# Kernel optimization log

Hardware: AMD Instinct MI355X
Metric: run time of the kernel (lower is better)

Reference implementation:

```python
import jax, jax.numpy as jnp
import numpy as np

B, S, D, H = 2, 2048, 1024, 16
Dh = D // H

def setup_inputs() -> dict:
    key = jax.random.key(0)
    ks = jax.random.split(key, 11)
    def lin(k, fan_in):
        bound = 1.0 / np.sqrt(fan_in)
        kw, kb = jax.random.split(k)
        W = jax.random.uniform(kw, (D, D), jnp.float32, -bound, bound)
        b = jax.random.uniform(kb, (D,), jnp.float32, -bound, bound)
        return W, b
    Wq, bq = lin(ks[0], D)
    Wk, bk = lin(ks[1], D)
    Wv, bv = lin(ks[2], D)
    Wo, bo = lin(ks[3], D)
    Q = jax.random.normal(ks[4], (B, S, D), jnp.float32)
    K = jax.random.normal(ks[5], (B, S, D), jnp.float32)
    V = jax.random.normal(ks[6], (B, S, D), jnp.float32)
    return {"Q": Q, "K": K, "V": V, "Wq": Wq, "bq": bq, "Wk": Wk, "bk": bk,
            "Wv": Wv, "bv": bv, "Wo": Wo, "bo": bo}

def _split_heads(x):
    # [B,S,D] -> [B,H,S,Dh]
    b, s, _ = x.shape
    return x.reshape(b, s, H, Dh).transpose(0, 2, 1, 3)

def reference(Q, K, V, Wq, bq, Wk, bk, Wv, bv, Wo, bo):
    q = _split_heads(Q @ Wq.T + bq)
    k = _split_heads(K @ Wk.T + bk)
    v = _split_heads(V @ Wv.T + bv)
    scores = jnp.einsum('bhqd,bhkd->bhqk', q, k) / jnp.sqrt(jnp.float32(Dh))
    attn = jax.nn.softmax(scores, axis=-1)
    out = jnp.einsum('bhqk,bhkd->bhqd', attn, v)  # [B,H,S,Dh]
    out = out.transpose(0, 2, 1, 3).reshape(Q.shape[0], Q.shape[1], D)
    return out @ Wo.T + bo
```

## Files before the change

kernel.cpp:

```cpp
#include <hip/hip_runtime.h>

#define SEQ 2048
#define DMODEL 1024
#define NH 16
#define DH 64

typedef __attribute__((ext_vector_type(8))) short bf16x8;
typedef __attribute__((ext_vector_type(4))) short bf16x4;
typedef __attribute__((ext_vector_type(4))) float floatx4;
typedef __attribute__((ext_vector_type(4))) unsigned short u16x4;
typedef unsigned short u16;
typedef unsigned int u32;

typedef const void __attribute__((address_space(1)))* as1cvp;
typedef void __attribute__((address_space(3)))* as3vp;

__device__ __forceinline__ void glds16(const void* g, void* l) {
    __builtin_amdgcn_global_load_lds((as1cvp)g, (as3vp)l, 16, 0, 0);
}

__device__ __forceinline__ u16 f2bf(float f) {
    union { u32 u; float f; } v; v.f = f;
    return (u16)((v.u + 0x8000u) >> 16);
}

__device__ __forceinline__ u32 pk2(float a, float b) {
    union { u32 u; float f; } x, y; x.f = a; y.f = b;
    u32 xr = x.u + 0x8000u, yr = y.u + 0x8000u;
#if __has_builtin(__builtin_amdgcn_perm)
    return __builtin_amdgcn_perm(yr, xr, 0x07060302u);
#else
    return (xr >> 16) | (yr & 0xffff0000u);
#endif
}

__device__ __forceinline__ float ex2(float x) {
#if __has_builtin(__builtin_amdgcn_exp2f)
    return __builtin_amdgcn_exp2f(x);
#else
    float r; asm("v_exp_f32 %0, %1" : "=v"(r) : "v"(x)); return r;
#endif
}

__device__ __forceinline__ floatx4 mfma32(bf16x8 a, bf16x8 b, floatx4 c) {
    return __builtin_amdgcn_mfma_f32_16x16x32_bf16(a, b, c, 0, 0, 0);
}

__device__ __forceinline__ uint4 cvt8(const float* __restrict__ p) {
    float4 a = *(const float4*)p;
    float4 b = *(const float4*)(p + 4);
    uint4 q;
    q.x = pk2(a.x, a.y); q.y = pk2(a.z, a.w);
    q.z = pk2(b.x, b.y); q.w = pk2(b.z, b.w);
    return q;
}

#define QSCALE 0.18033688011112042f

__global__ __launch_bounds__(256) void cvt_all(
    const float* __restrict__ Q, const float* __restrict__ K, const float* __restrict__ V,
    const float* __restrict__ W0, const float* __restrict__ W1,
    const float* __restrict__ W2, const float* __restrict__ W3,
    u16* __restrict__ Qb, u16* __restrict__ Kb, u16* __restrict__ Vb,
    u16* __restrict__ Wb)
{
    const int y = blockIdx.y;
    const float* src; u16* dst;
    if (y == 0)      { src = Q;  dst = Qb; }
    else if (y == 1) { src = K;  dst = Kb; }
    else if (y == 2) { src = V;  dst = Vb; }
    else {
        if (blockIdx.x >= 512) return;
        src = (y == 3) ? W0 : (y == 4) ? W1 : (y == 5) ? W2 : W3;
        dst = Wb + (size_t)(y - 3) * 1048576;
    }
    size_t i = ((size_t)blockIdx.x * 256 + threadIdx.x) * 8;
    *(uint4*)(dst + i) = cvt8(src + i);
}

__global__ __launch_bounds__(256) void cvt_w(
    const float* __restrict__ W0, const float* __restrict__ W1,
    const float* __restrict__ W2, const float* __restrict__ W3,
    u16* __restrict__ out)
{
    const float* src = (blockIdx.y == 0) ? W0 : (blockIdx.y == 1) ? W1
                     : (blockIdx.y == 2) ? W2 : W3;
    size_t i = ((size_t)blockIdx.x * 256 + threadIdx.x) * 8;
    *(uint4*)(out + (size_t)blockIdx.y * 1048576 + i) = cvt8(src + i);
}

__device__ __forceinline__ void qkv_store(
    int z, u16* __restrict__ outp, int rowg, int col, floatx4 a4, float bv, float sc)
{
    union { u32 w[2]; u16 h[4]; u16x4 v4; } pk;
    pk.w[0] = pk2((a4[0] + bv) * sc, (a4[1] + bv) * sc);
    pk.w[1] = pk2((a4[2] + bv) * sc, (a4[3] + bv) * sc);
    int b = rowg >> 11, s = rowg & 2047, h = col >> 6, d = col & 63;
    if (z < 2) {
#pragma unroll
        for (int r = 0; r < 4; r++)
            outp[((size_t)(b * NH + h) * SEQ + s + r) * DH + d] = pk.h[r];
    } else {
        *(u16x4*)(outp + ((size_t)(b * NH + h) * DH + d) * SEQ + s) = pk.v4;
    }
}

__global__ __launch_bounds__(256) void gemm_qkv_bb(
    const u16* __restrict__ Qb, const u16* __restrict__ Kb, const u16* __restrict__ Vb,
    const u16* __restrict__ Wb,
    const float* __restrict__ b0, const float* __restrict__ b1, const float* __restrict__ b2,
    u16* __restrict__ qo, u16* __restrict__ ko, u16* __restrict__ vto)
{
    __shared__ __align__(16) u16 As[3][4096];
    __shared__ __align__(16) u16 Bs[3][4096];
    const int tid = threadIdx.x, l = tid & 63, w = tid >> 6;
    const int lm = l & 15, quad = l >> 4;
    const int wr = (w >> 1) * 64, wc = (w & 1) * 64;
    const int bm = blockIdx.y * 128, bn = blockIdx.x * 128;
    const int z = blockIdx.z;
    const u16* A      = (z == 0) ? Qb : (z == 1) ? Kb : Vb;
    const u16* W      = Wb + (size_t)z * 1048576;
    const float* bias = (z == 0) ? b0 : (z == 1) ? b1 : b2;

    const int srow = tid >> 2, scol = (tid & 3) * 8;

    floatx4 acc[4][4];
#pragma unroll
    for (int i = 0; i < 4; i++)
#pragma unroll
        for (int j = 0; j < 4; j++) acc[i][j] = (floatx4){0.f, 0.f, 0.f, 0.f};

#define QKV_STAGE(I, NB) do { \
        const int kt_ = (I) * 32; \
        glds16(A + (size_t)(bm + srow) * DMODEL + kt_ + scol, As[NB] + w * 512); \
        glds16(A + (size_t)(bm + 64 + srow) * DMODEL + kt_ + scol, As[NB] + 2048 + w * 512); \
        glds16(W + (size_t)(bn + srow) * DMODEL + kt_ + scol, Bs[NB] + w * 512); \
        glds16(W + (size_t)(bn + 64 + srow) * DMODEL + kt_ + scol, Bs[NB] + 2048 + w * 512); \
    } while (0)

    QKV_STAGE(0, 0);
    QKV_STAGE(1, 1);
    asm volatile("s_waitcnt vmcnt(4)" ::: "memory");
    __builtin_amdgcn_s_barrier();

    int cur = 0, nx = 2;
    for (int i = 0; i < 32; i++) {
        bf16x8 af[4], bfr[4];
#pragma unroll
        for (int mi = 0; mi < 4; mi++)
            af[mi] = *(const bf16x8*)(As[cur] + (wr + mi * 16 + lm) * 32 + quad * 8);
#pragma unroll
        for (int ni = 0; ni < 4; ni++)
            bfr[ni] = *(const bf16x8*)(Bs[cur] + (wc + ni * 16 + lm) * 32 + quad * 8);
#pragma unroll
        for (int mi = 0; mi < 4; mi++)
#pragma unroll
            for (int ni = 0; ni < 4; ni++)
                acc[mi][ni] = __builtin_amdgcn_mfma_f32_16x16x32_bf16(
                    af[mi], bfr[ni], acc[mi][ni], 0, 0, 0);

        if (i + 2 < 32) {
            QKV_STAGE(i + 2, nx);
            asm volatile("s_waitcnt vmcnt(4)" ::: "memory");
            __builtin_amdgcn_s_barrier();
        } else if (i + 1 < 32) {
            asm volatile("s_waitcnt vmcnt(0)" ::: "memory");
            __builtin_amdgcn_s_barrier();
        }
        cur = (cur == 2) ? 0 : cur + 1;
        nx  = (nx == 2) ? 0 : nx + 1;
    }
#undef QKV_STAGE

    const float sc = (z == 0) ? QSCALE : 1.0f;
    u16* outp = (z == 0) ? qo : (z == 1) ? ko : vto;
#pragma unroll
    for (int ni = 0; ni < 4; ni++) {
        int col = bn + wc + ni * 16 + lm;
        float bv = bias[col];
#pragma unroll
        for (int mi = 0; mi < 4; mi++)
            qkv_store(z, outp, bm + wr + mi * 16 + quad * 4, col, acc[mi][ni], bv, sc);
    }
}

template<bool WBF>
__global__ __launch_bounds__(256) void gemm_qkv(
    const float* __restrict__ Qf, const float* __restrict__ Kf, const float* __restrict__ Vf,
    const void* __restrict__ W0, const void* __restrict__ W1, const void* __restrict__ W2,
    const float* __restrict__ b0, const float* __restrict__ b1, const float* __restrict__ b2,
    u16* __restrict__ qo, u16* __restrict__ ko, u16* __restrict__ vto)
{
    __shared__ __align__(16) u16 As[128 * 32];
    __shared__ __align__(16) u16 Bs[128 * 32];
    const int tid = threadIdx.x, l = tid & 63, w = tid >> 6;
    const int lm = l & 15, quad = l >> 4;
    const int wr = (w >> 1) * 64, wc = (w & 1) * 64;
    const int bm = blockIdx.y * 128, bn = blockIdx.x * 128;
    const int z = blockIdx.z;
    const float* A    = (z == 0) ? Qf : (z == 1) ? Kf : Vf;
    const void* Wp    = (z == 0) ? W0 : (z == 1) ? W1 : W2;
    const float* bias = (z == 0) ? b0 : (z == 1) ? b1 : b2;

    floatx4 acc[4][4];
#pragma unroll
    for (int i = 0; i < 4; i++)
#pragma unroll
        for (int j = 0; j < 4; j++) acc[i][j] = (floatx4){0.f, 0.f, 0.f, 0.f};

    for (int kt = 0; kt < DMODEL; kt += 32) {
        __syncthreads();
#pragma unroll
        for (int j = 0; j < 2; j++) {
            int ch = j * 256 + tid, row = ch >> 2, c = ch & 3;
            *(uint4*)(As + ch * 8) = cvt8(A + (size_t)(bm + row) * DMODEL + kt + c * 8);
        }
        if (WBF) {
            const u16* Wc = (const u16*)Wp;
            glds16(Wc + (size_t)(bn + (tid >> 2)) * DMODEL + kt + (tid & 3) * 8, Bs + w * 512);
            glds16(Wc + (size_t)(bn + 64 + (tid >> 2)) * DMODEL + kt + (tid & 3) * 8, Bs + 2048 + w * 512);
        } else {
            const float* Wf = (const float*)Wp;
#pragma unroll
            for (int j = 0; j < 2; j++) {
                int ch = j * 256 + tid, row = ch >> 2, c = ch & 3;
                *(uint4*)(Bs + ch * 8) = cvt8(Wf + (size_t)(bn + row) * DMODEL + kt + c * 8);
            }
        }
        __syncthreads();

        bf16x8 af[4], bfr[4];
#pragma unroll
        for (int mi = 0; mi < 4; mi++)
            af[mi] = *(const bf16x8*)(As + (wr + mi * 16 + lm) * 32 + quad * 8);
#pragma unroll
        for (int ni = 0; ni < 4; ni++)
            bfr[ni] = *(const bf16x8*)(Bs + (wc + ni * 16 + lm) * 32 + quad * 8);
#pragma unroll
        for (int mi = 0; mi < 4; mi++)
#pragma unroll
            for (int ni = 0; ni < 4; ni++)
                acc[mi][ni] = __builtin_amdgcn_mfma_f32_16x16x32_bf16(
                    af[mi], bfr[ni], acc[mi][ni], 0, 0, 0);
    }

    const float sc = (z == 0) ? QSCALE : 1.0f;
    u16* outp = (z == 0) ? qo : (z == 1) ? ko : vto;
#pragma unroll
    for (int ni = 0; ni < 4; ni++) {
        int col = bn + wc + ni * 16 + lm;
        float bv = bias[col];
#pragma unroll
        for (int mi = 0; mi < 4; mi++)
            qkv_store(z, outp, bm + wr + mi * 16 + quad * 4, col, acc[mi][ni], bv, sc);
    }
}

__global__ __launch_bounds__(256) void gemm_o_p(
    const u16* __restrict__ A, const u16* __restrict__ W,
    const float* __restrict__ bias, float* __restrict__ out)
{
    __shared__ __align__(16) u16 As[3][4096];
    __shared__ __align__(16) u16 Bs[3][2048];
    const int tid = threadIdx.x, l = tid & 63, w = tid >> 6;
    const int lm = l & 15, quad = l >> 4;
    const int bm = blockIdx.y * 128, bn = blockIdx.x * 64;

    floatx4 acc[2][4];
#pragma unroll
    for (int i = 0; i < 2; i++)
#pragma unroll
        for (int j = 0; j < 4; j++) acc[i][j] = (floatx4){0.f, 0.f, 0.f, 0.f};

#define O_STAGE(I, NB) do { \
        const int kt_ = (I) * 32; \
        glds16(A + (size_t)(bm + (tid >> 2)) * DMODEL + kt_ + (tid & 3) * 8, As[NB] + w * 512); \
        glds16(A + (size_t)(bm + 64 + (tid >> 2)) * DMODEL + kt_ + (tid & 3) * 8, As[NB] + 2048 + w * 512); \
        glds16(W + (size_t)(bn + (tid >> 2)) * DMODEL + kt_ + (tid & 3) * 8, Bs[NB] + w * 512); \
    } while (0)

    O_STAGE(0, 0);
    O_STAGE(1, 1);
    asm volatile("s_waitcnt vmcnt(3)" ::: "memory");
    __builtin_amdgcn_s_barrier();

    int cur = 0, nx = 2;
    for (int i = 0; i < 32; i++) {
        bf16x8 af[2], bfr[4];
#pragma unroll
        for (int mi = 0; mi < 2; mi++)
            af[mi] = *(const bf16x8*)(As[cur] + (w * 32 + mi * 16 + lm) * 32 + quad * 8);
#pragma unroll
        for (int ni = 0; ni < 4; ni++)
            bfr[ni] = *(const bf16x8*)(Bs[cur] + (ni * 16 + lm) * 32 + quad * 8);
#pragma unroll
        for (int mi = 0; mi < 2; mi++)
#pragma unroll
            for (int ni = 0; ni < 4; ni++)
                acc[mi][ni] = __builtin_amdgcn_mfma_f32_16x16x32_bf16(
                    af[mi], bfr[ni], acc[mi][ni], 0, 0, 0);

        if (i + 2 < 32) {
            O_STAGE(i + 2, nx);
            asm volatile("s_waitcnt vmcnt(3)" ::: "memory");
            __builtin_amdgcn_s_barrier();
        } else if (i + 1 < 32) {
            asm volatile("s_waitcnt vmcnt(0)" ::: "memory");
            __builtin_amdgcn_s_barrier();
        }
        cur = (cur == 2) ? 0 : cur + 1;
        nx  = (nx == 2) ? 0 : nx + 1;
    }
#undef O_STAGE

#pragma unroll
    for (int ni = 0; ni < 4; ni++) {
        int col = bn + ni * 16 + lm;
        float bv = bias[col];
#pragma unroll
        for (int mi = 0; mi < 2; mi++) {
#pragma unroll
            for (int r = 0; r < 4; r++) {
                int rowg = bm + w * 32 + mi * 16 + quad * 4 + r;
                out[(size_t)rowg * DMODEL + col] = acc[mi][ni][r] + bv;
            }
        }
    }
}

template<bool WBF>
__global__ __launch_bounds__(256) void gemm_o(
    const u16* __restrict__ A, const void* __restrict__ Wp,
    const float* __restrict__ bias, float* __restrict__ out)
{
    __shared__ __align__(16) u16 As[128 * 32];
    __shared__ __align__(16) u16 Bs[64 * 32];
    const int tid = threadIdx.x, l = tid & 63, w = tid >> 6;
    const int lm = l & 15, quad = l >> 4;
    const int bm = blockIdx.y * 128, bn = blockIdx.x * 64;

    floatx4 acc[2][4];
#pragma unroll
    for (int i = 0; i < 2; i++)
#pragma unroll
        for (int j = 0; j < 4; j++) acc[i][j] = (floatx4){0.f, 0.f, 0.f, 0.f};

    for (int kt = 0; kt < DMODEL; kt += 32) {
        __syncthreads();
        glds16(A + (size_t)(bm + (tid >> 2)) * DMODEL + kt + (tid & 3) * 8, As + w * 512);
        glds16(A + (size_t)(bm + 64 + (tid >> 2)) * DMODEL + kt + (tid & 3) * 8, As + 2048 + w * 512);
        if (WBF) {
            glds16((const u16*)Wp + (size_t)(bn + (tid >> 2)) * DMODEL + kt + (tid & 3) * 8, Bs + w * 512);
        } else {
            *(uint4*)(Bs + tid * 8) =
                cvt8((const float*)Wp + (size_t)(bn + (tid >> 2)) * DMODEL + kt + (tid & 3) * 8);
        }
        __syncthreads();

        bf16x8 af[2], bfr[4];
#pragma unroll
        for (int mi = 0; mi < 2; mi++)
            af[mi] = *(const bf16x8*)(As + (w * 32 + mi * 16 + lm) * 32 + quad * 8);
#pragma unroll
        for (int ni = 0; ni < 4; ni++)
            bfr[ni] = *(const bf16x8*)(Bs + (ni * 16 + lm) * 32 + quad * 8);
#pragma unroll
        for (int mi = 0; mi < 2; mi++)
#pragma unroll
            for (int ni = 0; ni < 4; ni++)
                acc[mi][ni] = __builtin_amdgcn_mfma_f32_16x16x32_bf16(
                    af[mi], bfr[ni], acc[mi][ni], 0, 0, 0);
    }

#pragma unroll
    for (int ni = 0; ni < 4; ni++) {
        int col = bn + ni * 16 + lm;
        float bv = bias[col];
#pragma unroll
        for (int mi = 0; mi < 2; mi++) {
#pragma unroll
            for (int r = 0; r < 4; r++) {
                int rowg = bm + w * 32 + mi * 16 + quad * 4 + r;
                out[(size_t)rowg * DMODEL + col] = acc[mi][ni][r] + bv;
            }
        }
    }
}

#define SP 72
#define TS (64 * SP)
#define BUFSZ (4 * TS)
__global__ __launch_bounds__(256, 2) void attn_kernel(
    const u16* __restrict__ q, const u16* __restrict__ k,
    const u16* __restrict__ vt, u16* __restrict__ out)
{
    __shared__ __align__(16) u16 smem[2 * BUFSZ];
    const int tid = threadIdx.x, l = tid & 63, w = tid >> 6;
    const int lm = l & 15, quad = l >> 4;
    const int qt = blockIdx.x, bh = blockIdx.y;
    const int b = bh >> 4, h = bh & 15;
    const int rg = w & 1, half = w >> 1;

    bf16x8 qf[4][2];
#pragma unroll
    for (int nt = 0; nt < 4; nt++) {
        int row = qt * 128 + rg * 64 + nt * 16 + lm;
        const u16* qp = q + ((size_t)bh * SEQ + row) * DH;
        qf[nt][0] = *(const bf16x8*)(qp + quad * 8);
        qf[nt][1] = *(const bf16x8*)(qp + 32 + quad * 8);
    }

    floatx4 O[4][4];
#pragma unroll
    for (int dt = 0; dt < 4; dt++)
#pragma unroll
        for (int nt = 0; nt < 4; nt++) O[dt][nt] = (floatx4){0.f, 0.f, 0.f, 0.f};
    floatx4 Ol[4];
#pragma unroll
    for (int nt = 0; nt < 4; nt++) Ol[nt] = (floatx4){0.f, 0.f, 0.f, 0.f};

    const bf16x8 ones8 = {(short)0x3F80, (short)0x3F80, (short)0x3F80, (short)0x3F80,
                          (short)0x3F80, (short)0x3F80, (short)0x3F80, (short)0x3F80};

    const int srow = tid >> 2, sc4 = tid & 3;
    const int prow = (srow & 32) | ((srow & 4) << 2) | ((srow & 24) >> 1) | (srow & 3);
    const u16* kbase = k + (size_t)bh * SEQ * DH;
    const u16* vbase = vt + (size_t)bh * DH * SEQ;

    uint4 kA0, kA1, kB0, kB1, vA0, vA1, vB0, vB1;
#define LOADT(T) do { \
        const u16* kgA = kbase + (size_t)((T) * 64 + srow) * DH + sc4 * 16; \
        const u16* kgB = kbase + (size_t)(1024 + (T) * 64 + srow) * DH + sc4 * 16; \
        kA0 = *(const uint4*)kgA;       kA1 = *(const uint4*)(kgA + 8); \
        kB0 = *(const uint4*)kgB;       kB1 = *(const uint4*)(kgB + 8); \
        const u16* vgA = vbase + (size_t)srow * SEQ + (T) * 64 + sc4 * 16; \
        const u16* vgB = vgA + 1024; \
        vA0 = *(const uint4*)vgA;       vA1 = *(const uint4*)(vgA + 8); \
        vB0 = *(const uint4*)vgB;       vB1 = *(const uint4*)(vgB + 8); \
    } while (0)
#define WRBUF(BUF) do { \
        u16* K0 = smem + (BUF) * BUFSZ; \
        u16* K1 = K0 + TS; \
        u16* V0 = K0 + 2 * TS; \
        u16* V1 = K0 + 3 * TS; \
        *(uint4*)(K0 + prow * SP + sc4 * 16)     = kA0; \
        *(uint4*)(K0 + prow * SP + sc4 * 16 + 8) = kA1; \
        *(uint4*)(K1 + prow * SP + sc4 * 16)     = kB0; \
        *(uint4*)(K1 + prow * SP + sc4 * 16 + 8) = kB1; \
        *(uint4*)(V0 + srow * SP + sc4 * 16)     = vA0; \
        *(uint4*)(V0 + srow * SP + sc4 * 16 + 8) = vA1; \
        *(uint4*)(V1 + srow * SP + sc4 * 16)     = vB0; \
        *(uint4*)(V1 + srow * SP + sc4 * 16 + 8) = vB1; \
    } while (0)

    LOADT(0);
    WRBUF(0);
    LOADT(1);
    asm volatile("s_waitcnt lgkmcnt(0)" ::: "memory");
    __builtin_amdgcn_s_barrier();

    for (int t = 0; t < 16; t++) {
        const int cur = t & 1;
        const u16* Kh = smem + cur * BUFSZ + half * TS;
        const u16* Vh = smem + cur * BUFSZ + (2 + half) * TS;

        floatx4 Sc[4][4];
        __builtin_amdgcn_s_setprio(1);
#pragma unroll
        for (int sub = 0; sub < 4; sub++) {
            bf16x8 ka0 = *(const bf16x8*)(Kh + (sub * 16 + lm) * SP + quad * 8);
            bf16x8 ka1 = *(const bf16x8*)(Kh + (sub * 16 + lm) * SP + 32 + quad * 8);
#pragma unroll
            for (int nt = 0; nt < 4; nt++) {
                floatx4 c = (floatx4){0.f, 0.f, 0.f, 0.f};
                c = mfma32(ka0, qf[nt][0], c);
                c = mfma32(ka1, qf[nt][1], c);
                Sc[sub][nt] = c;
            }
        }
        __builtin_amdgcn_s_setprio(0);

        if (t + 1 < 16) {
            asm volatile("s_waitcnt vmcnt(0)" ::: "memory");
            WRBUF(cur ^ 1);
            if (t + 2 < 16) LOADT(t + 2);
        }

        bf16x8 pbm[2][4];
#pragma unroll
        for (int p = 0; p < 2; p++)
#pragma unroll
            for (int nt = 0; nt < 4; nt++) {
                floatx4 sa = Sc[p * 2][nt], sb = Sc[p * 2 + 1][nt];
#pragma unroll
                for (int r = 0; r < 4; r++) { sa[r] = ex2(sa[r]); sb[r] = ex2(sb[r]); }
                union { u32 w4[4]; bf16x8 v; } pku;
                pku.w4[0] = pk2(sa[0], sa[1]);
                pku.w4[1] = pk2(sa[2], sa[3]);
                pku.w4[2] = pk2(sb[0], sb[1]);
                pku.w4[3] = pk2(sb[2], sb[3]);
                pbm[p][nt] = pku.v;
            }

        __builtin_amdgcn_s_setprio(1);
#pragma unroll
        for (int nt = 0; nt < 4; nt++) {
            Ol[nt] = mfma32(ones8, pbm[0][nt], Ol[nt]);
            Ol[nt] = mfma32(ones8, pbm[1][nt], Ol[nt]);
        }

#pragma unroll
        for (int dt = 0; dt < 4; dt++) {
            bf16x8 va0 = *(const bf16x8*)(Vh + (dt * 16 + lm) * SP + quad * 8);
            bf16x8 va1 = *(const bf16x8*)(Vh + (dt * 16 + lm) * SP + 32 + quad * 8);
#pragma unroll
            for (int nt = 0; nt < 4; nt++) {
                O[dt][nt] = mfma32(va0, pbm[0][nt], O[dt][nt]);
                O[dt][nt] = mfma32(va1, pbm[1][nt], O[dt][nt]);
            }
        }
        __builtin_amdgcn_s_setprio(0);

        asm volatile("s_waitcnt lgkmcnt(0)" ::: "memory");
        __builtin_amdgcn_s_barrier();
    }
#undef LOADT
#undef WRBUF

    float* obuf  = (float*)smem;
    float* mlbuf = (float*)smem + 8704;
    if (w >= 2) {
        float* ob = obuf + (rg * 64 + l) * 68;
        float* ml = mlbuf + (rg * 64 + l) * 5;
#pragma unroll
        for (int nt = 0; nt < 4; nt++) {
#pragma unroll
            for (int dt = 0; dt < 4; dt++)
                *(floatx4*)(ob + nt * 16 + dt * 4) = O[dt][nt];
            ml[nt] = Ol[nt][0];
        }
    }
    __syncthreads();
    if (w < 2) {
        float* ob = obuf + (rg * 64 + l) * 68;
        float* ml = mlbuf + (rg * 64 + l) * 5;
#pragma unroll
        for (int nt = 0; nt < 4; nt++) {
            float lB = ml[nt];
            float inv = 1.0f / (Ol[nt][0] + lB);
            int s = qt * 128 + rg * 64 + nt * 16 + lm;
            u16* op = out + ((size_t)b * SEQ + s) * DMODEL + h * DH;
#pragma unroll
            for (int dt = 0; dt < 4; dt++) {
                floatx4 Ob = *(const floatx4*)(ob + nt * 16 + dt * 4);
                union { u32 w2[2]; u16x4 v; } pku;
                pku.w2[0] = pk2((O[dt][nt][0] + Ob[0]) * inv,
                                (O[dt][nt][1] + Ob[1]) * inv);
                pku.w2[1] = pk2((O[dt][nt][2] + Ob[2]) * inv,
                                (O[dt][nt][3] + Ob[3]) * inv);
                *(u16x4*)(op + dt * 16 + quad * 4) = pku.v;
            }
        }
    }
}

extern "C" void kernel_launch(void* const* d_in, const int* in_sizes, int n_in,
                              void* d_out, int out_size, void* d_ws, size_t ws_size,
                              hipStream_t stream) {
    (void)in_sizes; (void)n_in; (void)out_size;
    const float* Q  = (const float*)d_in[0];
    const float* K  = (const float*)d_in[1];
    const float* V  = (const float*)d_in[2];
    const float* Wq = (const float*)d_in[3];
    const float* bq = (const float*)d_in[4];
    const float* Wk = (const float*)d_in[5];
    const float* bk = (const float*)d_in[6];
    const float* Wv = (const float*)d_in[7];
    const float* bv = (const float*)d_in[8];
    const float* Wo = (const float*)d_in[9];
    const float* bo = (const float*)d_in[10];

    const size_t NEL = (size_t)2 * NH * SEQ * DH;
    u16* base = (u16*)d_ws;
    dim3 bb(256);
    dim3 ab(256);

    if (ws_size >= 8 * NEL * 2) {
        u16* Qb   = base;
        u16* Kb   = Qb + NEL;
        u16* Vb   = Kb + NEL;
        u16* Wb   = Vb + NEL;
        u16* qws  = Wb + NEL;
        u16* kws  = qws + NEL;
        u16* vtws = kws + NEL;
        u16* aws  = vtws + NEL;
        cvt_all<<<dim3(2048, 7), bb, 0, stream>>>(Q, K, V, Wq, Wk, Wv, Wo, Qb, Kb, Vb, Wb);
        gemm_qkv_bb<<<dim3(8, 32, 3), bb, 0, stream>>>(
            Qb, Kb, Vb, Wb, bq, bk, bv, qws, kws, vtws);
        attn_kernel<<<dim3(SEQ / 128, 2 * NH), ab, 0, stream>>>(qws, kws, vtws, aws);
        gemm_o_p<<<dim3(16, 32), bb, 0, stream>>>(aws, Wb + 3145728, bo, (float*)d_out);
    } else if (ws_size >= 5 * NEL * 2) {
        u16* Wb = base;
        u16* qws = base + NEL; u16* kws = qws + NEL; u16* vtws = kws + NEL; u16* aws = vtws + NEL;
        cvt_w<<<dim3(512, 4), bb, 0, stream>>>(Wq, Wk, Wv, Wo, Wb);
        gemm_qkv<true><<<dim3(8, 32, 3), bb, 0, stream>>>(
            Q, K, V, Wb, Wb + 1048576, Wb + 2097152, bq, bk, bv, qws, kws, vtws);
        attn_kernel<<<dim3(SEQ / 128, 2 * NH), ab, 0, stream>>>(qws, kws, vtws, aws);
        gemm_o_p<<<dim3(16, 32), bb, 0, stream>>>(aws, Wb + 3145728, bo, (float*)d_out);
    } else {
        u16* qws = base; u16* kws = qws + NEL; u16* vtws = kws + NEL; u16* aws = vtws + NEL;
        gemm_qkv<false><<<dim3(8, 32, 3), bb, 0, stream>>>(
            Q, K, V, Wq, Wk, Wv, bq, bk, bv, qws, kws, vtws);
        attn_kernel<<<dim3(SEQ / 128, 2 * NH), ab, 0, stream>>>(qws, kws, vtws, aws);
        gemm_o<false><<<dim3(16, 32), bb, 0, stream>>>(aws, Wo, bo, (float*)d_out);
    }
}
```

Before: 218.7 us.

## Halve attention KV tile to 32 keys and raise occupancy to four blocks per CU

Shrinks each key/value tile per pipeline stage from 64 to 32 keys, which halves the shared-memory buffers and the S/P register arrays, and doubles the loop trip count to 32. The launch bound is raised from 2 to 4 blocks per CU to use the freed LDS and registers for more waves in flight, hiding latency. The cost is twice as many barriers and global-load rounds per block, with less MFMA work between each synchronization.

Result: slower. 484.9 us (+121.7%).

```diff
diff --git a/kernel.cpp b/kernel.cpp
--- a/kernel.cpp
+++ b/kernel.cpp
@@ -387,10 +387,13 @@
     }
 }
 
-#define SP 72
-#define TS (64 * SP)
-#define BUFSZ (4 * TS)
-__global__ __launch_bounds__(256, 2) void attn_kernel(
+#define KSP 72
+#define VSP 40
+#define KSZ (32 * KSP)
+#define VSZ (64 * VSP)
+#define BUFSZ (2 * KSZ + 2 * VSZ)
+#define NT 32
+__global__ __launch_bounds__(256, 4) void attn_kernel(
     const u16* __restrict__ q, const u16* __restrict__ k,
     const u16* __restrict__ vt, u16* __restrict__ out)
 {
@@ -422,35 +425,25 @@
     const bf16x8 ones8 = {(short)0x3F80, (short)0x3F80, (short)0x3F80, (short)0x3F80,
                           (short)0x3F80, (short)0x3F80, (short)0x3F80, (short)0x3F80};
 
-    const int srow = tid >> 2, sc4 = tid & 3;
-    const int prow = (srow & 32) | ((srow & 4) << 2) | ((srow & 24) >> 1) | (srow & 3);
+    const int krow = tid >> 3, kc = tid & 7;
+    const int vrow = tid >> 2, vc = tid & 3;
+    const int prow = ((krow & 4) << 2) | ((krow & 24) >> 1) | (krow & 3);
     const u16* kbase = k + (size_t)bh * SEQ * DH;
     const u16* vbase = vt + (size_t)bh * DH * SEQ;
 
-    uint4 kA0, kA1, kB0, kB1, vA0, vA1, vB0, vB1;
+    uint4 kA, kB, vA, vB;
 #define LOADT(T) do { \
-        const u16* kgA = kbase + (size_t)((T) * 64 + srow) * DH + sc4 * 16; \
-        const u16* kgB = kbase + (size_t)(1024 + (T) * 64 + srow) * DH + sc4 * 16; \
-        kA0 = *(const uint4*)kgA;       kA1 = *(const uint4*)(kgA + 8); \
-        kB0 = *(const uint4*)kgB;       kB1 = *(const uint4*)(kgB + 8); \
-        const u16* vgA = vbase + (size_t)srow * SEQ + (T) * 64 + sc4 * 16; \
-        const u16* vgB = vgA + 1024; \
-        vA0 = *(const uint4*)vgA;       vA1 = *(const uint4*)(vgA + 8); \
-        vB0 = *(const uint4*)vgB;       vB1 = *(const uint4*)(vgB + 8); \
+        kA = *(const uint4*)(kbase + (size_t)((T) * 32 + krow) * DH + kc * 8); \
+        kB = *(const uint4*)(kbase + (size_t)(1024 + (T) * 32 + krow) * DH + kc * 8); \
+        vA = *(const uint4*)(vbase + (size_t)vrow * SEQ + (T) * 32 + vc * 8); \
+        vB = *(const uint4*)(vbase + (size_t)vrow * SEQ + 1024 + (T) * 32 + vc * 8); \
     } while (0)
 #define WRBUF(BUF) do { \
-        u16* K0 = smem + (BUF) * BUFSZ; \
-        u16* K1 = K0 + TS; \
-        u16* V0 = K0 + 2 * TS; \
-        u16* V1 = K0 + 3 * TS; \
-        *(uint4*)(K0 + prow * SP + sc4 * 16)     = kA0; \
-        *(uint4*)(K0 + prow * SP + sc4 * 16 + 8) = kA1; \
-        *(uint4*)(K1 + prow * SP + sc4 * 16)     = kB0; \
-        *(uint4*)(K1 + prow * SP + sc4 * 16 + 8) = kB1; \
-        *(uint4*)(V0 + srow * SP + sc4 * 16)     = vA0; \
-        *(uint4*)(V0 + srow * SP + sc4 * 16 + 8) = vA1; \
-        *(uint4*)(V1 + srow * SP + sc4 * 16)     = vB0; \
-        *(uint4*)(V1 + srow * SP + sc4 * 16 + 8) = vB1; \
+        u16* B0 = smem + (BUF) * BUFSZ; \
+        *(uint4*)(B0 + prow * KSP + kc * 8)                 = kA; \
+        *(uint4*)(B0 + KSZ + prow * KSP + kc * 8)           = kB; \
+        *(uint4*)(B0 + 2 * KSZ + vrow * VSP + vc * 8)       = vA; \
+        *(uint4*)(B0 + 2 * KSZ + VSZ + vrow * VSP + vc * 8) = vB; \
     } while (0)
 
     LOADT(0);
@@ -459,17 +452,17 @@
     asm volatile("s_waitcnt lgkmcnt(0)" ::: "memory");
     __builtin_amdgcn_s_barrier();
 
-    for (int t = 0; t < 16; t++) {
+    for (int t = 0; t < NT; t++) {
         const int cur = t & 1;
-        const u16* Kh = smem + cur * BUFSZ + half * TS;
-        const u16* Vh = smem + cur * BUFSZ + (2 + half) * TS;
-
-        floatx4 Sc[4][4];
+        const u16* Kh = smem + cur * BUFSZ + half * KSZ;
+        const u16* Vh = smem + cur * BUFSZ + 2 * KSZ + half * VSZ;
+
+        floatx4 Sc[2][4];
         __builtin_amdgcn_s_setprio(1);
 #pragma unroll
-        for (int sub = 0; sub < 4; sub++) {
-            bf16x8 ka0 = *(const bf16x8*)(Kh + (sub * 16 + lm) * SP + quad * 8);
-            bf16x8 ka1 = *(const bf16x8*)(Kh + (sub * 16 + lm) * SP + 32 + quad * 8);
+        for (int sub = 0; sub < 2; sub++) {
+            bf16x8 ka0 = *(const bf16x8*)(Kh + (sub * 16 + lm) * KSP + quad * 8);
+            bf16x8 ka1 = *(const bf16x8*)(Kh + (sub * 16 + lm) * KSP + 32 + quad * 8);
 #pragma unroll
             for (int nt = 0; nt < 4; nt++) {
                 floatx4 c = (floatx4){0.f, 0.f, 0.f, 0.f};
@@ -480,44 +473,37 @@
         }
         __builtin_amdgcn_s_setprio(0);
 
-        if (t + 1 < 16) {
+        if (t + 1 < NT) {
             asm volatile("s_waitcnt vmcnt(0)" ::: "memory");
             WRBUF(cur ^ 1);
-            if (t + 2 < 16) LOADT(t + 2);
-        }
-
-        bf16x8 pbm[2][4];
-#pragma unroll
-        for (int p = 0; p < 2; p++)
-#pragma unroll
-            for (int nt = 0; nt < 4; nt++) {
-                floatx4 sa = Sc[p * 2][nt], sb = Sc[p * 2 + 1][nt];
-#pragma unroll
-                for (int r = 0; r < 4; r++) { sa[r] = ex2(sa[r]); sb[r] = ex2(sb[r]); }
-                union { u32 w4[4]; bf16x8 v; } pku;
-                pku.w4[0] = pk2(sa[0], sa[1]);
-                pku.w4[1] = pk2(sa[2], sa[3]);
-                pku.w4[2] = pk2(sb[0], sb[1]);
-                pku.w4[3] = pk2(sb[2], sb[3]);
-                pbm[p][nt] = pku.v;
-            }
+            if (t + 2 < NT) LOADT(t + 2);
+        }
+
+        bf16x8 pbm[4];
+#pragma unroll
+        for (int nt = 0; nt < 4; nt++) {
+            floatx4 sa = Sc[0][nt], sb = Sc[1][nt];
+#pragma unroll
+            for (int r = 0; r < 4; r++) { sa[r] = ex2(sa[r]); sb[r] = ex2(sb[r]); }
+            union { u32 w4[4]; bf16x8 v; } pku;
+            pku.w4[0] = pk2(sa[0], sa[1]);
+            pku.w4[1] = pk2(sa[2], sa[3]);
+            pku.w4[2] = pk2(sb[0], sb[1]);
+            pku.w4[3] = pk2(sb[2], sb[3]);
+            pbm[nt] = pku.v;
+        }
 
         __builtin_amdgcn_s_setprio(1);
 #pragma unroll
-        for (int nt = 0; nt < 4; nt++) {
-            Ol[nt] = mfma32(ones8, pbm[0][nt], Ol[nt]);
-            Ol[nt] = mfma32(ones8, pbm[1][nt], Ol[nt]);
-        }
+        for (int nt = 0; nt < 4; nt++)
+            Ol[nt] = mfma32(ones8, pbm[nt], Ol[nt]);
 
 #pragma unroll
         for (int dt = 0; dt < 4; dt++) {
-            bf16x8 va0 = *(const bf16x8*)(Vh + (dt * 16 + lm) * SP + quad * 8);
-            bf16x8 va1 = *(const bf16x8*)(Vh + (dt * 16 + lm) * SP + 32 + quad * 8);
-#pragma unroll
-            for (int nt = 0; nt < 4; nt++) {
-                O[dt][nt] = mfma32(va0, pbm[0][nt], O[dt][nt]);
-                O[dt][nt] = mfma32(va1, pbm[1][nt], O[dt][nt]);
-            }
+            bf16x8 va = *(const bf16x8*)(Vh + (dt * 16 + lm) * VSP + quad * 8);
+#pragma unroll
+            for (int nt = 0; nt < 4; nt++)
+                O[dt][nt] = mfma32(va, pbm[nt], O[dt][nt]);
         }
         __builtin_amdgcn_s_setprio(0);
 
```
